# Performance work log

Hardware: AMD Instinct MI355X
Metric: run time of the kernel (lower is better)

The kernel has to match this reference:

```python
import jax, jax.numpy as jnp
import numpy as np
from jax import lax

GRID = 200      # _FIXED_GRID_LEN
SOFT_K = 50.0   # _SOFT_MASK_K
BN_EPS = 1e-5


def setup_inputs() -> dict:
    key = jax.random.key(0)
    ks = jax.random.split(key, 12)
    B, L = 8192, 2001
    f32 = jnp.float32
    inp = {
        'phase': jax.random.uniform(ks[0], (B, L), f32, -1.0, 1.0),
        'primary_flux': 0.01 * jax.random.normal(ks[1], (B, L), f32),
        'secondary_flux': 0.01 * jax.random.normal(ks[2], (B, L), f32),
        'odd_even_diff': 0.01 * jax.random.normal(ks[3], (B, L), f32),
        # TaylorGateLayerV8 params
        'A': jnp.asarray(0.01, f32),
        'Bp': jnp.asarray(1.0, f32),
        't0': jnp.asarray(0.0, f32),
        # BatchNorm1d(4), eval mode (running stats)
        'bn_gamma': jnp.ones((4,), f32),
        'bn_beta': jnp.zeros((4,), f32),
        'bn_mean': jnp.zeros((4,), f32),
        'bn_var': jnp.ones((4,), f32),
        # Conv1d(4,8,7) / Conv1d(8,16,5)
        'conv1_w': 0.1 * jax.random.normal(ks[4], (8, 4, 7), f32),
        'conv1_b': jnp.zeros((8,), f32),
        'conv2_w': 0.1 * jax.random.normal(ks[5], (16, 8, 5), f32),
        'conv2_b': jnp.zeros((16,), f32),
        # Linear(21, 1)
        'fc_w': 0.1 * jax.random.normal(ks[6], (1, 21), f32),
        'fc_b': jnp.zeros((1,), f32),
    }
    return inp


def _conv1d(x, w, b, pad):
    # x: (B, C, L), w: (O, C, K)
    y = lax.conv_general_dilated(x, w, window_strides=(1,), padding=[(pad, pad)],
                                 dimension_numbers=('NCH', 'OIH', 'NCH'))
    return y + b[None, :, None]


def _interp_linear_ac(x, out_len):
    # torch F.interpolate(mode='linear', align_corners=True) on (B, L) -> (B, out_len)
    L = x.shape[1]
    pos = jnp.linspace(0.0, L - 1.0, out_len)
    i0 = jnp.floor(pos).astype(jnp.int32)
    i1 = jnp.minimum(i0 + 1, L - 1)
    w = (pos - i0).astype(x.dtype)
    return x[:, i0] * (1.0 - w) + x[:, i1] * w


def reference(phase, primary_flux, secondary_flux, odd_even_diff,
              A, Bp, t0, bn_gamma, bn_beta, bn_mean, bn_var,
              conv1_w, conv1_b, conv2_w, conv2_b, fc_w, fc_b):
    # --- TaylorGateLayerV8: 2nd-order Taylor U-shape transit template ---
    gate = -A * jnp.clip(1.0 - Bp * (phase - t0) ** 2, 0.0, None)

    # --- CNN branch ---
    x = jnp.stack([gate, primary_flux, secondary_flux, odd_even_diff], axis=1)  # (B,4,L)
    inv = bn_gamma / jnp.sqrt(bn_var + BN_EPS)
    x = x * inv[None, :, None] + (bn_beta - bn_mean * inv)[None, :, None]
    x = jax.nn.relu(_conv1d(x, conv1_w, conv1_b, 3))
    x = jax.nn.relu(_conv1d(x, conv2_w, conv2_b, 2))
    cnn_out = jnp.mean(x, axis=2)  # AdaptiveAvgPool1d(1) -> (B,16)

    # --- shape features ---
    batch = primary_flux.shape[0]
    A_abs = jnp.abs(A) + 1e-8
    depth = jnp.clip(-primary_flux, 0.0, None)
    depth_norm = depth / A_abs
    depth_rs = _interp_linear_ac(depth, GRID)  # (B, 200)
    dx = 2.0 / (GRID - 1)                       # trapz over linspace(-1,1,200)
    auc_raw = dx * (jnp.sum(depth_rs, axis=1) - 0.5 * (depth_rs[:, 0] + depth_rs[:, -1]))
    auc_norm = auc_raw / A_abs
    dip_all = jax.nn.sigmoid(SOFT_K * (depth_norm - 0.1))
    flat_bot = jax.nn.sigmoid(SOFT_K * (depth_norm - 0.8))
    ingress = dip_all - flat_bot
    total = 1.0 - dip_all + ingress + flat_bot + 1e-8
    ingress = ingress / total
    flat_bot = flat_bot / total
    t14 = jnp.mean(ingress + flat_bot, axis=1) + 1e-8
    t12_t14 = jnp.mean(ingress, axis=1) / t14
    flat_bottom = jnp.mean(flat_bot, axis=1)
    B_bcast = jnp.broadcast_to(Bp, (batch,)).astype(depth.dtype)
    shape = jnp.stack([B_bcast, auc_raw, auc_norm, t12_t14, flat_bottom], axis=1)  # (B,5)

    features = jnp.concatenate([cnn_out, shape], axis=1)  # (B,21)
    logits = features @ fc_w.T + fc_b
    return jax.nn.sigmoid(logits)
```

## Files before the change

### kernel.cpp

```cpp
#include <hip/hip_runtime.h>
#include <math.h>

#define L_LEN 2001
#define CCH 1024
#define XREC 1056
#define NT1 65
#define NT2 64

typedef __attribute__((ext_vector_type(8))) short bf16x8;
typedef __attribute__((ext_vector_type(4))) float f32x4;

union FragU { unsigned u[4]; bf16x8 v; };

__device__ __forceinline__ unsigned short f2bf(float f) {
    unsigned u = __builtin_bit_cast(unsigned, f);
    u += 0x7fffu + ((u >> 16) & 1u);
    return (unsigned short)(u >> 16);
}
__device__ __forceinline__ unsigned bfpack(float lo, float hi) {
    unsigned ul = __builtin_bit_cast(unsigned, lo);
    unsigned uh = __builtin_bit_cast(unsigned, hi);
    ul += 0x7fffu + ((ul >> 16) & 1u);
    uh += 0x7fffu + ((uh >> 16) & 1u);
    return __builtin_amdgcn_perm(uh, ul, 0x07060302);
}
__device__ __forceinline__ float fast_rcp(float x) { return __builtin_amdgcn_rcpf(x); }
__device__ __forceinline__ float sigmf(float x) { return fast_rcp(1.0f + __expf(-x)); }

__global__ __launch_bounds__(256, 6)
void taylor_cnn_v8_mfma(const float* __restrict__ phase, const float* __restrict__ primary,
                        const float* __restrict__ secondary, const float* __restrict__ oddeven,
                        const float* __restrict__ pA, const float* __restrict__ pBp,
                        const float* __restrict__ pT0,
                        const float* __restrict__ bng, const float* __restrict__ bnb,
                        const float* __restrict__ bnm, const float* __restrict__ bnv,
                        const float* __restrict__ w1, const float* __restrict__ b1,
                        const float* __restrict__ w2, const float* __restrict__ b2,
                        const float* __restrict__ fcw, const float* __restrict__ fcb,
                        float* __restrict__ out, int nrows)
{
    __shared__ __align__(16) unsigned int xs_i[XREC * 2];
    __shared__ __align__(16) unsigned int y1_i[XREC * 4];
    __shared__ float redA[4][16];
    __shared__ float redB[4][3];

    const int tid = threadIdx.x;
    const int row = blockIdx.x;
    if (row >= nrows) return;
    const long base = (long)row * L_LEN;

    const int lane = tid & 63;
    const int wid  = tid >> 6;
    const int n    = lane & 15;
    const int quad = lane >> 4;

    const float A  = pA[0];
    const float Bp = pBp[0];
    const float t0 = pT0[0];
    const float A_abs = fabsf(A) + 1e-8f;
    const float rAabs = 1.0f / A_abs;

    float inv[4], off[4];
#pragma unroll
    for (int c = 0; c < 4; ++c) {
        float iv = bng[c] / sqrtf(bnv[c] + 1e-5f);
        inv[c] = iv;
        off[c] = bnb[c] - bnm[c] * iv;
    }

    bf16x8 a1;
#pragma unroll
    for (int jp = 0; jp < 8; ++jp) {
        int j = quad + 4 * (jp >> 2);
        int c = jp & 3;
        float v = (n < 8 && j < 7) ? w1[(n * 4 + c) * 7 + j] : 0.0f;
        a1[jp] = (short)f2bf(v);
    }
    bf16x8 a20, a21;
#pragma unroll
    for (int jp = 0; jp < 8; ++jp) {
        float v0 = w2[(n * 8 + jp) * 5 + quad];
        float v1 = (quad + 4 < 5) ? w2[(n * 8 + jp) * 5 + quad + 4] : 0.0f;
        a20[jp] = (short)f2bf(v0);
        a21[jp] = (short)f2bf(v1);
    }
    float b1v[4], b2v[4];
#pragma unroll
    for (int r = 0; r < 4; ++r) {
        b1v[r] = b1[(quad * 4 + r) & 7];
        b2v[r] = b2[quad * 4 + r];
    }

    float s_ing = 0.0f, s_fb = 0.0f;
    float m0 = 0.f, m1 = 0.f, m2 = 0.f, m3 = 0.f;
    const f32x4 fz = {0.f, 0.f, 0.f, 0.f};

    auto stageA = [&](int c0) {
        for (int m = tid; m < XREC; m += 256) {
            int p = c0 + m - 16;
            unsigned d0 = 0u, d1 = 0u;
            if (p >= 0 && p < L_LEN) {
                float ph = phase[base + p];
                float pf = primary[base + p];
                float sf = secondary[base + p];
                float oe = oddeven[base + p];
                float dd = ph - t0;
                float gate = -A * fmaxf(1.0f - Bp * dd * dd, 0.0f);
                d0 = bfpack(gate * inv[0] + off[0], pf * inv[1] + off[1]);
                d1 = bfpack(sf   * inv[2] + off[2], oe * inv[3] + off[3]);
                if (m >= 16 && m < 16 + CCH) {
                    float depth = fmaxf(-pf, 0.0f);
                    float dn  = depth * rAabs;
                    float dip = sigmf(50.0f * (dn - 0.1f));
                    float fb  = sigmf(50.0f * (dn - 0.8f));
                    float ing = dip - fb;
                    float tot = 1.0f - dip + ing + fb + 1e-8f;
                    float rt  = fast_rcp(tot);
                    s_ing += ing * rt;
                    s_fb  += fb  * rt;
                }
            }
            *(uint2*)&xs_i[2 * m] = make_uint2(d0, d1);
        }
    };

    auto stageB = [&](int c0) {
        for (int t = wid; t < NT1; t += 4) {
            int qb = 16 * t + n + quad + 5;
            uint2 lo = *(const uint2*)&xs_i[2 * qb];
            uint2 hi = *(const uint2*)&xs_i[2 * (qb + 4)];
            FragU bu; bu.u[0] = lo.x; bu.u[1] = lo.y; bu.u[2] = hi.x; bu.u[3] = hi.y;
            f32x4 d = __builtin_amdgcn_mfma_f32_16x16x32_bf16(a1, bu.v, fz, 0, 0, 0);
            if (lane < 32) {
                int p = c0 - 8 + 16 * t + n;
                bool ok = (p >= 0 && p < L_LEN);
                unsigned w0 = 0u, w1_ = 0u;
                if (ok) {
                    w0  = bfpack(fmaxf(d[0] + b1v[0], 0.f), fmaxf(d[1] + b1v[1], 0.f));
                    w1_ = bfpack(fmaxf(d[2] + b1v[2], 0.f), fmaxf(d[3] + b1v[3], 0.f));
                }
                *(uint2*)&y1_i[4 * (16 * t + n) + 2 * quad] = make_uint2(w0, w1_);
            }
        }
    };

    auto stageC = [&](int c0) {
        for (int t = wid; t < NT2; t += 4) {
            int q = 16 * t + n + quad + 6;
            uint4 r0 = *(const uint4*)&y1_i[4 * q];
            uint4 r1 = *(const uint4*)&y1_i[4 * (q + 4)];
            FragU u0, u1;
            u0.u[0] = r0.x; u0.u[1] = r0.y; u0.u[2] = r0.z; u0.u[3] = r0.w;
            u1.u[0] = r1.x; u1.u[1] = r1.y; u1.u[2] = r1.z; u1.u[3] = r1.w;
            f32x4 d = __builtin_amdgcn_mfma_f32_16x16x32_bf16(a20, u0.v, fz, 0, 0, 0);
            d = __builtin_amdgcn_mfma_f32_16x16x32_bf16(a21, u1.v, d, 0, 0, 0);
            int p = c0 + 16 * t + n;
            float msk = (p < L_LEN) ? 1.0f : 0.0f;
            m0 = fmaf(fmaxf(d[0] + b2v[0], 0.f), msk, m0);
            m1 = fmaf(fmaxf(d[1] + b2v[1], 0.f), msk, m1);
            m2 = fmaf(fmaxf(d[2] + b2v[2], 0.f), msk, m2);
            m3 = fmaf(fmaxf(d[3] + b2v[3], 0.f), msk, m3);
        }
    };

    float s_auc = 0.0f;
    if (tid < 200) {
        float pos = (float)tid * (2000.0f / 199.0f);
        int i0 = (int)pos;
        if (i0 > 2000) i0 = 2000;
        int i1 = (i0 + 1 < L_LEN) ? i0 + 1 : 2000;
        float w  = pos - (float)i0;
        float d0 = fmaxf(-primary[base + i0], 0.f);
        float d1 = fmaxf(-primary[base + i1], 0.f);
        float v  = d0 * (1.0f - w) + d1 * w;
        float wt = (tid == 0 || tid == 199) ? 0.5f : 1.0f;
        s_auc = v * wt;
    }

    stageA(0);
    __syncthreads();
    stageB(0);
    __syncthreads();
    stageA(CCH);
    stageC(0);
    __syncthreads();
    stageB(CCH);
    __syncthreads();
    stageC(CCH);

#pragma unroll
    for (int dlt = 8; dlt >= 1; dlt >>= 1) {
        m0 += __shfl_xor(m0, dlt);
        m1 += __shfl_xor(m1, dlt);
        m2 += __shfl_xor(m2, dlt);
        m3 += __shfl_xor(m3, dlt);
    }
    if ((lane & 15) == 0) {
        redA[wid][quad * 4 + 0] = m0;
        redA[wid][quad * 4 + 1] = m1;
        redA[wid][quad * 4 + 2] = m2;
        redA[wid][quad * 4 + 3] = m3;
    }
#pragma unroll
    for (int dlt = 32; dlt >= 1; dlt >>= 1) {
        s_ing += __shfl_xor(s_ing, dlt);
        s_fb  += __shfl_xor(s_fb,  dlt);
        s_auc += __shfl_xor(s_auc, dlt);
    }
    if (lane == 0) {
        redB[wid][0] = s_ing;
        redB[wid][1] = s_fb;
        redB[wid][2] = s_auc;
    }
    __syncthreads();

    if (tid == 0) {
        float logit = fcb[0];
#pragma unroll
        for (int oc = 0; oc < 16; ++oc) {
            float s = redA[0][oc] + redA[1][oc] + redA[2][oc] + redA[3][oc];
            logit += (s / 2001.0f) * fcw[oc];
        }
        float Sing = redB[0][0] + redB[1][0] + redB[2][0] + redB[3][0];
        float Sfb  = redB[0][1] + redB[1][1] + redB[2][1] + redB[3][1];
        float Sauc = redB[0][2] + redB[1][2] + redB[2][2] + redB[3][2];

        float auc_raw  = (float)(2.0 / 199.0) * Sauc;
        float auc_norm = auc_raw / A_abs;
        float m_ing = Sing / 2001.0f;
        float m_fb  = Sfb  / 2001.0f;
        float t14   = (Sing + Sfb) / 2001.0f + 1e-8f;
        float t12   = m_ing / t14;

        logit += Bp       * fcw[16]
               + auc_raw  * fcw[17]
               + auc_norm * fcw[18]
               + t12      * fcw[19]
               + m_fb     * fcw[20];

        out[row] = 1.0f / (1.0f + expf(-logit));
    }
}

extern "C" void kernel_launch(void* const* d_in, const int* in_sizes, int n_in,
                              void* d_out, int out_size, void* d_ws, size_t ws_size,
                              hipStream_t stream) {
    const float* phase     = (const float*)d_in[0];
    const float* primary   = (const float*)d_in[1];
    const float* secondary = (const float*)d_in[2];
    const float* oddeven   = (const float*)d_in[3];
    const float* pA        = (const float*)d_in[4];
    const float* pBp       = (const float*)d_in[5];
    const float* pT0       = (const float*)d_in[6];
    const float* bng       = (const float*)d_in[7];
    const float* bnb       = (const float*)d_in[8];
    const float* bnm       = (const float*)d_in[9];
    const float* bnv       = (const float*)d_in[10];
    const float* w1        = (const float*)d_in[11];
    const float* b1        = (const float*)d_in[12];
    const float* w2        = (const float*)d_in[13];
    const float* b2        = (const float*)d_in[14];
    const float* fcw       = (const float*)d_in[15];
    const float* fcb       = (const float*)d_in[16];
    float* out = (float*)d_out;

    int nrows = in_sizes[0] / L_LEN;
    dim3 grid(nrows), block(256);
    hipLaunchKernelGGL(taylor_cnn_v8_mfma, grid, block, 0, stream,
                       phase, primary, secondary, oddeven, pA, pBp, pT0,
                       bng, bnb, bnm, bnv, w1, b1, w2, b2, fcw, fcb, out, nrows);
}
```

Before: 315.3 us.

## Specialize stage loops per chunk, simplify soft-mask math, fold biases into MFMA

Unrolls the input staging into per-chunk variants so only boundary records pay bounds checks and clamping. Second-chunk conv loops are trimmed to the tiles that cover valid positions, and output masking is restricted to the straddling tile. The two sigmoids are rewritten as a single exp2 with reciprocal forms, and the total-normalisation reciprocal is dropped as algebraically redundant. Biases are passed as the MFMA accumulator, and a hardware packed bf16 conversion is used when available. This risks subtle numeric differences from exp overflow behaviour and hardcoded tile indices.

```diff
diff --git a/kernel.cpp b/kernel.cpp
--- a/kernel.cpp
+++ b/kernel.cpp
@@ -4,13 +4,14 @@
 #define L_LEN 2001
 #define CCH 1024
 #define XREC 1056
-#define NT1 65
-#define NT2 64
 
 typedef __attribute__((ext_vector_type(8))) short bf16x8;
 typedef __attribute__((ext_vector_type(4))) float f32x4;
-
-union FragU { unsigned u[4]; bf16x8 v; };
+#if __has_builtin(__builtin_amdgcn_cvt_pk_bf16_f32)
+typedef __attribute__((ext_vector_type(2))) __bf16 bf16x2_t;
+#endif
+
+union FragU { unsigned u[4]; uint2 u2[2]; uint4 u4; bf16x8 v; };
 
 __device__ __forceinline__ unsigned short f2bf(float f) {
     unsigned u = __builtin_bit_cast(unsigned, f);
@@ -18,14 +19,25 @@
     return (unsigned short)(u >> 16);
 }
 __device__ __forceinline__ unsigned bfpack(float lo, float hi) {
+#if __has_builtin(__builtin_amdgcn_cvt_pk_bf16_f32)
+    bf16x2_t r = __builtin_amdgcn_cvt_pk_bf16_f32(lo, hi);
+    return __builtin_bit_cast(unsigned, r);
+#else
     unsigned ul = __builtin_bit_cast(unsigned, lo);
     unsigned uh = __builtin_bit_cast(unsigned, hi);
     ul += 0x7fffu + ((ul >> 16) & 1u);
     uh += 0x7fffu + ((uh >> 16) & 1u);
     return __builtin_amdgcn_perm(uh, ul, 0x07060302);
+#endif
 }
 __device__ __forceinline__ float fast_rcp(float x) { return __builtin_amdgcn_rcpf(x); }
-__device__ __forceinline__ float sigmf(float x) { return fast_rcp(1.0f + __expf(-x)); }
+__device__ __forceinline__ float fexp2(float x) {
+#if __has_builtin(__builtin_amdgcn_exp2f)
+    return __builtin_amdgcn_exp2f(x);
+#else
+    return __expf(x * 0.69314718f);
+#endif
+}
 
 __global__ __launch_bounds__(256, 6)
 void taylor_cnn_v8_mfma(const float* __restrict__ phase, const float* __restrict__ primary,
@@ -46,7 +58,6 @@
 
     const int tid = threadIdx.x;
     const int row = blockIdx.x;
-    if (row >= nrows) return;
     const long base = (long)row * L_LEN;
 
     const int lane = tid & 63;
@@ -59,13 +70,21 @@
     const float t0 = pT0[0];
     const float A_abs = fabsf(A) + 1e-8f;
     const float rAabs = 1.0f / A_abs;
-
-    float inv[4], off[4];
-#pragma unroll
-    for (int c = 0; c < 4; ++c) {
-        float iv = bng[c] / sqrtf(bnv[c] + 1e-5f);
-        inv[c] = iv;
-        off[c] = bnb[c] - bnm[c] * iv;
+    const float nBp  = -Bp;
+    const float cExp = -72.134766f * rAabs;
+
+    float inv1, inv2, inv3, gInv0, off0, off1, off2, off3;
+    {
+        float iv0 = bng[0] / sqrtf(bnv[0] + 1e-5f);
+        float iv1 = bng[1] / sqrtf(bnv[1] + 1e-5f);
+        float iv2 = bng[2] / sqrtf(bnv[2] + 1e-5f);
+        float iv3 = bng[3] / sqrtf(bnv[3] + 1e-5f);
+        gInv0 = -A * iv0;
+        inv1 = iv1; inv2 = iv2; inv3 = iv3;
+        off0 = bnb[0] - bnm[0] * iv0;
+        off1 = bnb[1] - bnm[1] * iv1;
+        off2 = bnb[2] - bnm[2] * iv2;
+        off3 = bnb[3] - bnm[3] * iv3;
     }
 
     bf16x8 a1;
@@ -84,84 +103,15 @@
         a20[jp] = (short)f2bf(v0);
         a21[jp] = (short)f2bf(v1);
     }
-    float b1v[4], b2v[4];
+    f32x4 cb1, cb2;
 #pragma unroll
     for (int r = 0; r < 4; ++r) {
-        b1v[r] = b1[(quad * 4 + r) & 7];
-        b2v[r] = b2[quad * 4 + r];
+        cb1[r] = b1[(quad * 4 + r) & 7];
+        cb2[r] = b2[quad * 4 + r];
     }
 
     float s_ing = 0.0f, s_fb = 0.0f;
     float m0 = 0.f, m1 = 0.f, m2 = 0.f, m3 = 0.f;
-    const f32x4 fz = {0.f, 0.f, 0.f, 0.f};
-
-    auto stageA = [&](int c0) {
-        for (int m = tid; m < XREC; m += 256) {
-            int p = c0 + m - 16;
-            unsigned d0 = 0u, d1 = 0u;
-            if (p >= 0 && p < L_LEN) {
-                float ph = phase[base + p];
-                float pf = primary[base + p];
-                float sf = secondary[base + p];
-                float oe = oddeven[base + p];
-                float dd = ph - t0;
-                float gate = -A * fmaxf(1.0f - Bp * dd * dd, 0.0f);
-                d0 = bfpack(gate * inv[0] + off[0], pf * inv[1] + off[1]);
-                d1 = bfpack(sf   * inv[2] + off[2], oe * inv[3] + off[3]);
-                if (m >= 16 && m < 16 + CCH) {
-                    float depth = fmaxf(-pf, 0.0f);
-                    float dn  = depth * rAabs;
-                    float dip = sigmf(50.0f * (dn - 0.1f));
-                    float fb  = sigmf(50.0f * (dn - 0.8f));
-                    float ing = dip - fb;
-                    float tot = 1.0f - dip + ing + fb + 1e-8f;
-                    float rt  = fast_rcp(tot);
-                    s_ing += ing * rt;
-                    s_fb  += fb  * rt;
-                }
-            }
-            *(uint2*)&xs_i[2 * m] = make_uint2(d0, d1);
-        }
-    };
-
-    auto stageB = [&](int c0) {
-        for (int t = wid; t < NT1; t += 4) {
-            int qb = 16 * t + n + quad + 5;
-            uint2 lo = *(const uint2*)&xs_i[2 * qb];
-            uint2 hi = *(const uint2*)&xs_i[2 * (qb + 4)];
-            FragU bu; bu.u[0] = lo.x; bu.u[1] = lo.y; bu.u[2] = hi.x; bu.u[3] = hi.y;
-            f32x4 d = __builtin_amdgcn_mfma_f32_16x16x32_bf16(a1, bu.v, fz, 0, 0, 0);
-            if (lane < 32) {
-                int p = c0 - 8 + 16 * t + n;
-                bool ok = (p >= 0 && p < L_LEN);
-                unsigned w0 = 0u, w1_ = 0u;
-                if (ok) {
-                    w0  = bfpack(fmaxf(d[0] + b1v[0], 0.f), fmaxf(d[1] + b1v[1], 0.f));
-                    w1_ = bfpack(fmaxf(d[2] + b1v[2], 0.f), fmaxf(d[3] + b1v[3], 0.f));
-                }
-                *(uint2*)&y1_i[4 * (16 * t + n) + 2 * quad] = make_uint2(w0, w1_);
-            }
-        }
-    };
-
-    auto stageC = [&](int c0) {
-        for (int t = wid; t < NT2; t += 4) {
-            int q = 16 * t + n + quad + 6;
-            uint4 r0 = *(const uint4*)&y1_i[4 * q];
-            uint4 r1 = *(const uint4*)&y1_i[4 * (q + 4)];
-            FragU u0, u1;
-            u0.u[0] = r0.x; u0.u[1] = r0.y; u0.u[2] = r0.z; u0.u[3] = r0.w;
-            u1.u[0] = r1.x; u1.u[1] = r1.y; u1.u[2] = r1.z; u1.u[3] = r1.w;
-            f32x4 d = __builtin_amdgcn_mfma_f32_16x16x32_bf16(a20, u0.v, fz, 0, 0, 0);
-            d = __builtin_amdgcn_mfma_f32_16x16x32_bf16(a21, u1.v, d, 0, 0, 0);
-            int p = c0 + 16 * t + n;
-            float msk = (p < L_LEN) ? 1.0f : 0.0f;
-            m0 = fmaf(fmaxf(d[0] + b2v[0], 0.f), msk, m0);
-            m1 = fmaf(fmaxf(d[1] + b2v[1], 0.f), msk, m1);
-            m2 = fmaf(fmaxf(d[2] + b2v[2], 0.f), msk, m2);
-            m3 = fmaf(fmaxf(d[3] + b2v[3], 0.f), msk, m3);
-        }
-    };
 
     float s_auc = 0.0f;
     if (tid < 200) {
@@ -177,16 +127,108 @@
         s_auc = v * wt;
     }
 
-    stageA(0);
-    __syncthreads();
-    stageB(0);
-    __syncthreads();
-    stageA(CCH);
-    stageC(0);
-    __syncthreads();
-    stageB(CCH);
-    __syncthreads();
-    stageC(CCH);
+    auto aRec = [&](int m, int p, bool chk) {
+        bool valid = true, core = true;
+        int pc = p;
+        if (chk) {
+            valid = ((unsigned)p < (unsigned)L_LEN);
+            core  = valid && (m >= 16) && (m < 16 + CCH);
+            pc = min(max(p, 0), L_LEN - 1);
+        }
+        float ph = phase[base + pc];
+        float pf = primary[base + pc];
+        float sf = secondary[base + pc];
+        float oe = oddeven[base + pc];
+        float dd = ph - t0;
+        float g  = fmaxf(fmaf(dd * dd, nBp, 1.0f), 0.0f);
+        float x0 = fmaf(g,  gInv0, off0);
+        float x1 = fmaf(pf, inv1, off1);
+        float x2 = fmaf(sf, inv2, off2);
+        float x3 = fmaf(oe, inv3, off3);
+        unsigned d0 = bfpack(x0, x1);
+        unsigned d1 = bfpack(x2, x3);
+        if (chk && !valid) { d0 = 0u; d1 = 0u; }
+        *(uint2*)&xs_i[2 * m] = make_uint2(d0, d1);
+        float depth = fmaxf(-pf, 0.0f);
+        float e   = fexp2(depth * cExp);
+        float dip = fast_rcp(fmaf(e, 148.413159f, 1.0f));
+        float fb  = fast_rcp(fmaf(e, 2.35385267e17f, 1.0f));
+        float ing = dip - fb;
+        if (chk && !core) { ing = 0.f; fb = 0.f; }
+        s_ing += ing;
+        s_fb  += fb;
+    };
+
+    auto stageA0 = [&]() {
+        aRec(tid, tid - 16, true);
+#pragma unroll
+        for (int k = 1; k < 4; ++k) aRec(tid + 256 * k, tid + 256 * k - 16, false);
+        if (tid < 32) aRec(1024 + tid, 1008 + tid, true);
+    };
+    auto stageA1 = [&]() {
+        aRec(tid, 1008 + tid, true);
+#pragma unroll
+        for (int k = 1; k < 3; ++k) aRec(tid + 256 * k, 1008 + tid + 256 * k, false);
+        aRec(tid + 768, 1776 + tid, true);
+    };
+
+    auto stageB = [&](int c0, int nt, int straddle_t) {
+        for (int t = wid; t < nt; t += 4) {
+            int qb = 16 * t + n + quad + 5;
+            FragU bu;
+            bu.u2[0] = *(const uint2*)&xs_i[2 * qb];
+            bu.u2[1] = *(const uint2*)&xs_i[2 * (qb + 4)];
+            f32x4 d = __builtin_amdgcn_mfma_f32_16x16x32_bf16(a1, bu.v, cb1, 0, 0, 0);
+            if (lane < 32) {
+                int q = 16 * t + n;
+                unsigned w0, w1_;
+                if (t == straddle_t) {
+                    int p = c0 - 8 + q;
+                    bool ok = ((unsigned)p < (unsigned)L_LEN);
+                    w0  = ok ? bfpack(fmaxf(d[0], 0.f), fmaxf(d[1], 0.f)) : 0u;
+                    w1_ = ok ? bfpack(fmaxf(d[2], 0.f), fmaxf(d[3], 0.f)) : 0u;
+                } else {
+                    w0  = bfpack(fmaxf(d[0], 0.f), fmaxf(d[1], 0.f));
+                    w1_ = bfpack(fmaxf(d[2], 0.f), fmaxf(d[3], 0.f));
+                }
+                *(uint2*)&y1_i[4 * q + 2 * quad] = make_uint2(w0, w1_);
+            }
+        }
+    };
+
+    auto stageC = [&](int nt, bool maskLast) {
+        for (int t = wid; t < nt; t += 4) {
+            int q = 16 * t + n + quad + 6;
+            FragU u0, u1;
+            u0.u4 = *(const uint4*)&y1_i[4 * q];
+            u1.u4 = *(const uint4*)&y1_i[4 * (q + 4)];
+            f32x4 d = __builtin_amdgcn_mfma_f32_16x16x32_bf16(a20, u0.v, cb2, 0, 0, 0);
+            d = __builtin_amdgcn_mfma_f32_16x16x32_bf16(a21, u1.v, d, 0, 0, 0);
+            if (maskLast && t == 61) {
+                float msk = (n == 0) ? 1.0f : 0.0f;
+                m0 = fmaf(fmaxf(d[0], 0.f), msk, m0);
+                m1 = fmaf(fmaxf(d[1], 0.f), msk, m1);
+                m2 = fmaf(fmaxf(d[2], 0.f), msk, m2);
+                m3 = fmaf(fmaxf(d[3], 0.f), msk, m3);
+            } else {
+                m0 += fmaxf(d[0], 0.f);
+                m1 += fmaxf(d[1], 0.f);
+                m2 += fmaxf(d[2], 0.f);
+                m3 += fmaxf(d[3], 0.f);
+            }
+        }
+    };
+
+    stageA0();
+    __syncthreads();
+    stageB(0, 65, 0);
+    __syncthreads();
+    stageA1();
+    stageC(64, false);
+    __syncthreads();
+    stageB(1024, 62, 61);
+    __syncthreads();
+    stageC(62, true);
 
 #pragma unroll
     for (int dlt = 8; dlt >= 1; dlt >>= 1) {
```

New measurement: 301.5 us. 1.05x faster.
